# Optimization experiments

Measured on AMD Instinct MI355X. Metric: run time of the kernel, lower is better.

## Reference

```python
import jax, jax.numpy as jnp
import numpy as np

# Static DAG: input -> L hidden layers of K nodes (dense between layers) -> output.
B, WIDTH, K, L = 262144, 64, 4, 4


def _linear_init(key, shape, fan_in):
    # matches nn.Linear default: U(-1/sqrt(fan_in), 1/sqrt(fan_in))
    bound = 1.0 / np.sqrt(fan_in)
    return jax.random.uniform(key, shape, jnp.float32, -bound, bound)


def setup_inputs() -> dict:
    key = jax.random.key(0)
    ks = jax.random.split(key, 9)
    x = jax.random.normal(ks[0], (B, WIDTH), jnp.float32)
    # input node -> first hidden layer (K edges)
    W_in = _linear_init(ks[1], (K, WIDTH, WIDTH), WIDTH)
    b_in = _linear_init(ks[2], (K, WIDTH), WIDTH)
    # between hidden layers: (L-1) transitions, K*K edges each; [pred, node, out, in]
    W_mid = _linear_init(ks[3], (L - 1, K, K, WIDTH, WIDTH), WIDTH)
    b_mid = _linear_init(ks[4], (L - 1, K, K, WIDTH), WIDTH)
    # last hidden layer -> output node (K edges)
    W_out = _linear_init(ks[5], (K, WIDTH, WIDTH), WIDTH)
    b_out = _linear_init(ks[6], (K, WIDTH), WIDTH)
    return {"x": x, "W_in": W_in, "b_in": b_in, "W_mid": W_mid,
            "b_mid": b_mid, "W_out": W_out, "b_out": b_out}


def _l2_normalize(t):
    # torch.linalg.norm(t) with no dim: Frobenius norm over the WHOLE tensor
    return t / jnp.linalg.norm(t)


def reference(x, W_in, b_in, W_mid, b_mid, W_out, b_out):
    # input node -> layer 1: each node k gets a single edge Linear, then normalize
    h = jnp.einsum('bw,kvw->kbv', x, W_in) + b_in[:, None, :]  # [K,B,W]
    h = jax.vmap(_l2_normalize)(h)
    # hidden -> hidden transitions: node v sums over its K predecessor edges
    for l in range(L - 1):  # small fixed structural loop over layers
        pre = jnp.einsum('pbw,pkvw->kbv', h, W_mid[l]) + b_mid[l].sum(axis=0)[:, None, :]
        h = jax.vmap(_l2_normalize)(pre)
    # last layer -> output node: sum K edge outputs, normalize
    out = jnp.einsum('pbw,pvw->bv', h, W_out) + b_out.sum(axis=0)
    return _l2_normalize(out)
```

## Files before the change

kernel.cpp:

```cpp
#include <hip/hip_runtime.h>


#define BF 262144.0f

#define OFF_G     0
#define OFF_S     4096
#define OFF_Q1    4160
#define OFF_Q2    4224
#define OFF_Q3    4288
#define OFF_Q4    5312
#define OFF_N2    21696
#define OFF_COUT  21760
#define OFF_SV1   21824
#define OFF_SV2   22080
#define OFF_SV3   23104
#define OFF_SV4   27200
#define OFF_MO    43584
#define OFF_P2    49152
#define OFF_P3    114688
#define OFF_P4    376832
#define OFF_PO    1425408
#define OFF_X16   2473984
#define NZERO     17600

typedef __attribute__((ext_vector_type(8))) short bf16x8;
typedef __attribute__((ext_vector_type(4))) float f32x4;
typedef __attribute__((ext_vector_type(4))) unsigned short u16x4;

__device__ __forceinline__ unsigned short f2bf(float f) {
  unsigned u = __builtin_bit_cast(unsigned, f);
  u += 0x7FFF + ((u >> 16) & 1);
  return (unsigned short)(u >> 16);
}

__device__ __forceinline__ bf16x8 cvt8(f32x4 a, f32x4 b, float s) {
  bf16x8 t;
#pragma unroll
  for (int j = 0; j < 4; j++) {
    t[j]     = (short)f2bf(a[j] * s);
    t[j + 4] = (short)f2bf(b[j] * s);
  }
  return t;
}

__device__ __forceinline__ void ld64(float* dst, const float* __restrict__ src, int tid) {
#pragma unroll
  for (int m = 0; m < 4; m++) {
    const int li = m * 1024 + tid * 4;
    *(f32x4*)&dst[(li >> 6) * 68 + (li & 63)] = *(const f32x4*)(src + li);
  }
}
__device__ __forceinline__ void st64(float* __restrict__ dst, const float* src, int tid) {
#pragma unroll
  for (int m = 0; m < 4; m++) {
    const int li = m * 1024 + tid * 4;
    *(f32x4*)(dst + li) = *(const f32x4*)&src[(li >> 6) * 68 + (li & 63)];
  }
}
__device__ __forceinline__ void mm64(float* C, const float* A, const float* B, int tid) {
  const int v0 = (tid >> 4) * 4, w0 = (tid & 15) * 4;
  f32x4 a0 = {0.f,0.f,0.f,0.f}, a1 = a0, a2 = a0, a3 = a0;
#pragma unroll 8
  for (int u = 0; u < 64; u++) {
    const f32x4 b = *(const f32x4*)&B[u * 68 + w0];
    a0 += b * A[(v0 + 0) * 68 + u];
    a1 += b * A[(v0 + 1) * 68 + u];
    a2 += b * A[(v0 + 2) * 68 + u];
    a3 += b * A[(v0 + 3) * 68 + u];
  }
  *(f32x4*)&C[(v0 + 0) * 68 + w0] = a0;
  *(f32x4*)&C[(v0 + 1) * 68 + w0] = a1;
  *(f32x4*)&C[(v0 + 2) * 68 + w0] = a2;
  *(f32x4*)&C[(v0 + 3) * 68 + w0] = a3;
}

__global__ __launch_bounds__(256) void kGP(const float* __restrict__ x,
                                           float* __restrict__ Gpart,
                                           unsigned short* __restrict__ x16,
                                           const float* __restrict__ Win,
                                           const float* __restrict__ Wmid,
                                           const float* __restrict__ Wout,
                                           float* __restrict__ ws) {
  __shared__ __align__(16) char shm[3 * 4352 * 4];
  const int tid = threadIdx.x;

  if (blockIdx.x < 512) {
    typedef unsigned short xts_t[4][16][8];
    xts_t* xts = (xts_t*)shm;
    float (*sred)[4] = (float(*)[4])(shm + 4096);
    const int lane = tid & 63, mt = tid >> 6;
    const int col = lane & 15, q = lane >> 4;
    const int row0 = tid >> 4;
    const int cf0  = (tid & 15) * 4;

    f32x4 acc[4];
#pragma unroll
    for (int nt = 0; nt < 4; nt++) acc[nt] = (f32x4){0.f, 0.f, 0.f, 0.f};
    float s0 = 0.f, s1 = 0.f, s2 = 0.f, s3 = 0.f;

    const long brow = (long)blockIdx.x * 512;
    const float* bx = x + brow * 64;
    f32x4 r0 = *(const f32x4*)(bx + tid * 4);
    f32x4 r1 = *(const f32x4*)(bx + 1024 + tid * 4);

    for (int c = 0; c < 16; c++) {
      __syncthreads();
      s0 += r0[0] + r1[0]; s1 += r0[1] + r1[1];
      s2 += r0[2] + r1[2]; s3 += r0[3] + r1[3];
      u16x4 h0, h1;
#pragma unroll
      for (int j = 0; j < 4; j++) {
        const int cf = cf0 + j;
        const unsigned short b0 = f2bf(r0[j]);
        const unsigned short b1 = f2bf(r1[j]);
        h0[j] = b0; h1[j] = b1;
        xts[cf >> 4][row0 >> 3][cf & 15][row0 & 7]        = b0;
        xts[cf >> 4][2 + (row0 >> 3)][cf & 15][row0 & 7]  = b1;
      }
      *(u16x4*)(x16 + (brow + c * 32 + row0) * 64 + cf0)      = h0;
      *(u16x4*)(x16 + (brow + c * 32 + 16 + row0) * 64 + cf0) = h1;
      f32x4 r0n = r0, r1n = r1;
      if (c < 15) {
        r0n = *(const f32x4*)(bx + (c + 1) * 2048 + tid * 4);
        r1n = *(const f32x4*)(bx + (c + 1) * 2048 + 1024 + tid * 4);
      }
      __syncthreads();
      const bf16x8 af = *(const bf16x8*)xts[mt][q][col];
#pragma unroll
      for (int nt = 0; nt < 4; nt++) {
        const bf16x8 bfr = *(const bf16x8*)xts[nt][q][col];
        acc[nt] = __builtin_amdgcn_mfma_f32_16x16x32_bf16(af, bfr, acc[nt], 0, 0, 0);
      }
      r0 = r0n; r1 = r1n;
    }

    float* myp = Gpart + (long)blockIdx.x * 4160;
#pragma unroll
    for (int nt = 0; nt < 4; nt++)
#pragma unroll
      for (int r = 0; r < 4; r++)
        myp[(mt * 16 + q * 4 + r) * 64 + nt * 16 + col] = acc[nt][r];

    sred[tid][0] = s0; sred[tid][1] = s1; sred[tid][2] = s2; sred[tid][3] = s3;
    __syncthreads();
    if (tid < 64) {
      float t = 0.f;
#pragma unroll
      for (int k2 = 0; k2 < 16; k2++) t += sred[(tid >> 2) + 16 * k2][tid & 3];
      myp[4096 + tid] = t;
    }
  } else {
    float* mb0 = (float*)shm;
    float* mb1 = mb0 + 4352;
    float* mb2 = mb1 + 4352;
    const int pid = blockIdx.x - 512;
    const int p1 = (pid >> 6) & 3, p2 = (pid >> 4) & 3, p3 = (pid >> 2) & 3, p4 = pid & 3;
    ld64(mb0, Win + p1 * 4096, tid);
    ld64(mb1, Wmid + (p1 * 4 + p2) * 4096, tid);
    __syncthreads();
    mm64(mb2, mb1, mb0, tid);
    __syncthreads();
    if (p3 == 0 && p4 == 0) st64(ws + OFF_P2 + (p1 * 4 + p2) * 4096, mb2, tid);
    ld64(mb1, Wmid + 65536 + (p2 * 4 + p3) * 4096, tid);
    __syncthreads();
    mm64(mb0, mb1, mb2, tid);
    __syncthreads();
    if (p4 == 0) st64(ws + OFF_P3 + (p1 * 16 + p2 * 4 + p3) * 4096, mb0, tid);
    ld64(mb1, Wmid + 131072 + (p3 * 4 + p4) * 4096, tid);
    __syncthreads();
    mm64(mb2, mb1, mb0, tid);
    __syncthreads();
    st64(ws + OFF_P4 + pid * 4096, mb2, tid);
    ld64(mb1, Wout + p4 * 4096, tid);
    __syncthreads();
    mm64(mb0, mb1, mb2, tid);
    __syncthreads();
    st64(ws + OFF_PO + pid * 4096, mb0, tid);
  }
}

__global__ __launch_bounds__(256) void kGred(const float* __restrict__ Gpart,
                                             float* __restrict__ ws) {
  __shared__ float red[4][64];
  const int tid = threadIdx.x;
  for (int i = blockIdx.x * 256 + tid; i < NZERO; i += 65 * 256)
    ws[OFF_Q1 + i] = 0.f;
  const int e = blockIdx.x * 64 + (tid & 63);
  const int quarter = tid >> 6;
  float acc = 0.f;
#pragma unroll 4
  for (int j = 0; j < 128; j++)
    acc += Gpart[(long)(quarter * 128 + j) * 4160 + e];
  red[quarter][tid & 63] = acc;
  __syncthreads();
  if (tid < 64) {
    const float t = red[0][tid] + red[1][tid] + red[2][tid] + red[3][tid];
    const int ee = blockIdx.x * 64 + tid;
    if (ee < 4096) ws[OFF_G + ee] = t;
    else           ws[OFF_S + ee - 4096] = t;
  }
}

__global__ __launch_bounds__(256) void kTab(const float* __restrict__ Win,
                                            float* __restrict__ ws) {
  __shared__ __align__(16) float Gl[64 * 68];
  __shared__ __align__(16) float Al[64 * 68];
  __shared__ __align__(16) float Bl[64 * 68];
  __shared__ float red[256];
  __shared__ float sl[64];
  const int tid = threadIdx.x, b = blockIdx.x;
  const int it = tid >> 6, lane = tid & 63;

  ld64(Gl, ws + OFF_G, tid);
  if (tid < 64) sl[tid] = ws[OFF_S + tid];
  __syncthreads();

  if (b < 4) {
    ld64(Al, Win + b * 4096, tid);
    __syncthreads();
    const int vq = it, w = lane;
    float part = 0.f;
    for (int m = 0; m < 16; m++) {
      const int v = vq + m * 4;
      float bw = 0.f;
#pragma unroll 8
      for (int wp = 0; wp < 64; wp++) bw += Al[v * 68 + wp] * Gl[wp * 68 + w];
      part += bw * Al[v * 68 + w];
    }
    red[tid] = part;
    __syncthreads();
    for (int st = 128; st > 0; st >>= 1) {
      if (tid < st) red[tid] += red[tid + st];
      __syncthreads();
    }
    if (tid == 0) ws[OFF_Q1 + b] = red[0];
  } else if (b < 164) {
    int NP, nv, v0, node, qoff;
    const float* Pbase;
    if (b < 20)      { NP = 4;  node = (b - 4)  >> 2; v0 = ((b - 4)  & 3) * 16; nv = 16; Pbase = ws + OFF_P2; qoff = OFF_Q2 + node * 16; }
    else if (b < 36) { NP = 16; node = (b - 20) >> 2; v0 = ((b - 20) & 3) * 16; nv = 16; Pbase = ws + OFF_P3; qoff = OFF_Q3 + node * 256; }
    else             { NP = 64; node = (b - 36) >> 5; v0 = ((b - 36) & 31) * 2; nv = 2;  Pbase = ws + OFF_P4; qoff = OFF_Q4 + node * 4096; }

    float q1acc = 0.f;
    f32x4 qq0 = {0.f,0.f,0.f,0.f}, qq1 = qq0, qq2 = qq0, qq3 = qq0;

    for (int vi = 0; vi < nv; vi++) {
      const int v = v0 + vi;
      __syncthreads();
      for (int e = tid * 4; e < NP * 64; e += 1024) {
        const int j = e >> 6, c = e & 63;
        *(f32x4*)&Al[j * 68 + c] = *(const f32x4*)(Pbase + (long)(j * 4 + node) * 4096 + v * 64 + c);
      }
      __syncthreads();
      if (NP == 64) {
        const int j = tid >> 2, w0 = (tid & 3) * 16;
        f32x4 a0 = {0.f,0.f,0.f,0.f}, a1 = a0, a2 = a0, a3 = a0;
#pragma unroll 8
        for (int wp = 0; wp < 64; wp++) {
          const float a = Al[j * 68 + wp];
          a0 += a * *(const f32x4*)&Gl[wp * 68 + w0];
          a1 += a * *(const f32x4*)&Gl[wp * 68 + w0 + 4];
          a2 += a * *(const f32x4*)&Gl[wp * 68 + w0 + 8];
          a3 += a * *(const f32x4*)&Gl[wp * 68 + w0 + 12];
        }
        *(f32x4*)&Bl[j * 68 + w0]      = a0;
        *(f32x4*)&Bl[j * 68 + w0 + 4]  = a1;
        *(f32x4*)&Bl[j * 68 + w0 + 8]  = a2;
        *(f32x4*)&Bl[j * 68 + w0 + 12] = a3;
      } else if (NP == 16) {
        const int j = tid >> 4, w0 = (tid & 15) * 4;
        f32x4 a0 = {0.f,0.f,0.f,0.f};
#pragma unroll 8
        for (int wp = 0; wp < 64; wp++)
          a0 += Al[j * 68 + wp] * *(const f32x4*)&Gl[wp * 68 + w0];
        *(f32x4*)&Bl[j * 68 + w0] = a0;
      } else {
        const int j = tid >> 6, w = tid & 63;
        float a0 = 0.f;
#pragma unroll 8
        for (int wp = 0; wp < 64; wp++) a0 += Al[j * 68 + wp] * Gl[wp * 68 + w];
        Bl[j * 68 + w] = a0;
      }
      __syncthreads();
      if (NP == 64) {
        const int j0 = (tid >> 4) * 4, jp = tid & 15;
#pragma unroll 4
        for (int w4 = 0; w4 < 16; w4++) {
          const f32x4 b0 = *(const f32x4*)&Bl[(j0 + 0) * 68 + w4 * 4];
          const f32x4 b1 = *(const f32x4*)&Bl[(j0 + 1) * 68 + w4 * 4];
          const f32x4 b2 = *(const f32x4*)&Bl[(j0 + 2) * 68 + w4 * 4];
          const f32x4 b3 = *(const f32x4*)&Bl[(j0 + 3) * 68 + w4 * 4];
#pragma unroll
          for (int bb = 0; bb < 4; bb++) {
            const f32x4 av = *(const f32x4*)&Al[(jp + 16 * bb) * 68 + w4 * 4];
            qq0[bb] += b0[0]*av[0] + b0[1]*av[1] + b0[2]*av[2] + b0[3]*av[3];
            qq1[bb] += b1[0]*av[0] + b1[1]*av[1] + b1[2]*av[2] + b1[3]*av[3];
            qq2[bb] += b2[0]*av[0] + b2[1]*av[1] + b2[2]*av[2] + b2[3]*av[3];
            qq3[bb] += b3[0]*av[0] + b3[1]*av[1] + b3[2]*av[2] + b3[3]*av[3];
          }
        }
      } else if (NP == 16) {
        const int j = tid >> 4, jp = tid & 15;
#pragma unroll 4
        for (int w4 = 0; w4 < 16; w4++) {
          const f32x4 bv = *(const f32x4*)&Bl[j * 68 + w4 * 4];
          const f32x4 av = *(const f32x4*)&Al[jp * 68 + w4 * 4];
          q1acc += bv[0]*av[0] + bv[1]*av[1] + bv[2]*av[2] + bv[3]*av[3];
        }
      } else {
        if (tid < 16) {
          const int j = tid >> 2, jp = tid & 3;
#pragma unroll 8
          for (int w = 0; w < 64; w++) q1acc += Bl[j * 68 + w] * Al[jp * 68 + w];
        }
      }
    }
    if (NP == 64) {
      const int j0 = (tid >> 4) * 4, jp = tid & 15;
#pragma unroll
      for (int bb = 0; bb < 4; bb++) {
        atomicAdd(&ws[qoff + (j0 + 0) * 64 + jp + 16 * bb], qq0[bb]);
        atomicAdd(&ws[qoff + (j0 + 1) * 64 + jp + 16 * bb], qq1[bb]);
        atomicAdd(&ws[qoff + (j0 + 2) * 64 + jp + 16 * bb], qq2[bb]);
        atomicAdd(&ws[qoff + (j0 + 3) * 64 + jp + 16 * bb], qq3[bb]);
      }
    } else if (NP == 16) {
      atomicAdd(&ws[qoff + (tid >> 4) * 16 + (tid & 15)], q1acc);
    } else if (tid < 16) {
      atomicAdd(&ws[qoff + tid], q1acc);
    }
  } else {
    const int vb = b - 164;
    const int lo = vb * 85, hi = (vb == 3) ? 340 : lo + 85;
    for (int vec = lo + it; vec < hi; vec += 4) {
      const float* mat; int dst;
      if (vec < 4)       { mat = Win + vec * 4096;                dst = OFF_SV1 + vec * 64; }
      else if (vec < 20) { mat = ws + OFF_P2 + (vec - 4) * 4096;  dst = OFF_SV2 + (vec - 4) * 64; }
      else if (vec < 84) { mat = ws + OFF_P3 + (vec - 20) * 4096; dst = OFF_SV3 + (vec - 20) * 64; }
      else               { mat = ws + OFF_P4 + (vec - 84) * 4096; dst = OFF_SV4 + (vec - 84) * 64; }
      float acc = 0.f;
#pragma unroll
      for (int u4 = 0; u4 < 16; u4++) {
        const f32x4 mv = *(const f32x4*)(mat + lane * 64 + u4 * 4);
        acc += mv[0]*sl[u4*4] + mv[1]*sl[u4*4+1] + mv[2]*sl[u4*4+2] + mv[3]*sl[u4*4+3];
      }
      ws[dst + lane] = acc;
    }
  }
}

__global__ __launch_bounds__(256) void kLM(
    const float* __restrict__ bin, const float* __restrict__ Wmid,
    const float* __restrict__ bmid, const float* __restrict__ Wout,
    const float* __restrict__ bout, float* __restrict__ ws) {
  __shared__ float binl[256], c2l[256], c3l[256], c4l[256], col[64];
  __shared__ float sv1l[256], sv2l[1024];
  __shared__ float inv1[4], inv2[4], inv3[4], inv4[4];
  __shared__ float C2l[4], C3l[16], C4l[64], mco[256];
  __shared__ __align__(16) float Grow[64 * 68];
  __shared__ float sl[64];
  __shared__ float tfl[4][64];
  __shared__ float redb[256];
  const int tid = threadIdx.x, it = tid >> 6, lane = tid & 63;

  binl[tid] = bin[tid];
  sv1l[tid] = ws[OFF_SV1 + tid];
#pragma unroll
  for (int m = 0; m < 4; m++) sv2l[m * 256 + tid] = ws[OFF_SV2 + m * 256 + tid];
  if (tid < 64) sl[tid] = ws[OFF_S + tid];
  ld64(Grow, ws + OFF_G, tid);
  __syncthreads();

  {
    const float c = binl[it * 64 + lane];
    float part = c * (2.f * sv1l[it * 64 + lane] + BF * c);
#pragma unroll
    for (int off = 32; off; off >>= 1) part += __shfl_down(part, off, 64);
    if (lane == 0) inv1[it] = rsqrtf(ws[OFF_Q1 + it] + part);
  }
  __syncthreads();
  if (tid < 4) C2l[tid] = inv1[tid];
  __syncthreads();
  {
    float acc = 0.f;
#pragma unroll
    for (int src = 0; src < 4; src++) {
      const float* wr = Wmid + (long)((src * 4 + it) * 64 + lane) * 64;
      float pc = 0.f;
#pragma unroll
      for (int u4 = 0; u4 < 16; u4++) {
        const f32x4 wv = *(const f32x4*)(wr + u4 * 4);
        pc += wv[0]*binl[src*64+u4*4]   + wv[1]*binl[src*64+u4*4+1]
            + wv[2]*binl[src*64+u4*4+2] + wv[3]*binl[src*64+u4*4+3];
      }
      acc += inv1[src] * pc + bmid[(src * 4 + it) * 64 + lane];
    }
    c2l[it * 64 + lane] = acc;
  }
  __syncthreads();
  {
    float ts = 0.f;
#pragma unroll
    for (int p1 = 0; p1 < 4; p1++) ts += C2l[p1] * sv2l[(p1 * 4 + it) * 64 + lane];
    const float c = c2l[it * 64 + lane];
    float part = c * (2.f * ts + BF * c);
    if (lane < 16) part += C2l[lane >> 2] * C2l[lane & 3] * ws[OFF_Q2 + it * 16 + lane];
#pragma unroll
    for (int off = 32; off; off >>= 1) part += __shfl_down(part, off, 64);
    if (lane == 0) inv2[it] = rsqrtf(part);
  }
  __syncthreads();
  if (tid < 16) C3l[tid] = C2l[tid >> 2] * inv2[tid & 3];
  __syncthreads();
  {
    float acc = 0.f;
#pragma unroll
    for (int src = 0; src < 4; src++) {
      const float* wr = Wmid + 65536 + (long)((src * 4 + it) * 64 + lane) * 64;
      float pc = 0.f;
#pragma unroll
      for (int u4 = 0; u4 < 16; u4++) {
        const f32x4 wv = *(const f32x4*)(wr + u4 * 4);
        pc += wv[0]*c2l[src*64+u4*4]   + wv[1]*c2l[src*64+u4*4+1]
            + wv[2]*c2l[src*64+u4*4+2] + wv[3]*c2l[src*64+u4*4+3];
      }
      acc += inv2[src] * pc + bmid[1024 + (src * 4 + it) * 64 + lane];
    }
    c3l[it * 64 + lane] = acc;
  }
  __syncthreads();
  {
    float ts = 0.f;
#pragma unroll
    for (int j = 0; j < 16; j++) ts += C3l[j] * ws[OFF_SV3 + (j * 4 + it) * 64 + lane];
    const float c = c3l[it * 64 + lane];
    float part = c * (2.f * ts + BF * c);
#pragma unroll
    for (int k = 0; k < 4; k++) {
      const int idx = lane * 4 + k;
      part += C3l[idx >> 4] * C3l[idx & 15] * ws[OFF_Q3 + it * 256 + idx];
    }
#pragma unroll
    for (int off = 32; off; off >>= 1) part += __shfl_down(part, off, 64);
    if (lane == 0) inv3[it] = rsqrtf(part);
  }
  __syncthreads();
  if (tid < 64) C4l[tid] = C3l[tid >> 2] * inv3[tid & 3];
  __syncthreads();
  {
    float acc = 0.f;
#pragma unroll
    for (int src = 0; src < 4; src++) {
      const float* wr = Wmid + 131072 + (long)((src * 4 + it) * 64 + lane) * 64;
      float pc = 0.f;
#pragma unroll
      for (int u4 = 0; u4 < 16; u4++) {
        const f32x4 wv = *(const f32x4*)(wr + u4 * 4);
        pc += wv[0]*c3l[src*64+u4*4]   + wv[1]*c3l[src*64+u4*4+1]
            + wv[2]*c3l[src*64+u4*4+2] + wv[3]*c3l[src*64+u4*4+3];
      }
      acc += inv3[src] * pc + bmid[2048 + (src * 4 + it) * 64 + lane];
    }
    c4l[it * 64 + lane] = acc;
  }
  __syncthreads();
  {
    float ts = 0.f;
    for (int j = 0; j < 64; j++) ts += C4l[j] * ws[OFF_SV4 + (j * 4 + it) * 64 + lane];
    const float c = c4l[it * 64 + lane];
    float part = c * (2.f * ts + BF * c);
    float rsum = 0.f;
    const float* qrow = ws + OFF_Q4 + it * 4096 + lane * 64;
#pragma unroll 8
    for (int jp = 0; jp < 64; jp++) rsum += C4l[jp] * qrow[jp];
    part += C4l[lane] * rsum;
#pragma unroll
    for (int off = 32; off; off >>= 1) part += __shfl_down(part, off, 64);
    if (lane == 0) inv4[it] = rsqrtf(part);
  }
  __syncthreads();
  mco[tid] = C4l[tid >> 2] * inv4[tid & 3];
  {
    const float* wr = Wout + (long)(it * 64 + lane) * 64;
    float pc = 0.f;
#pragma unroll
    for (int u4 = 0; u4 < 16; u4++) {
      const f32x4 wv = *(const f32x4*)(wr + u4 * 4);
      pc += wv[0]*c4l[it*64+u4*4]   + wv[1]*c4l[it*64+u4*4+1]
          + wv[2]*c4l[it*64+u4*4+2] + wv[3]*c4l[it*64+u4*4+3];
    }
    c2l[it * 64 + lane] = inv4[it] * pc + bout[it * 64 + lane];
  }
  __syncthreads();
  if (tid < 64) col[tid] = c2l[tid] + c2l[64 + tid] + c2l[128 + tid] + c2l[192 + tid];
  __syncthreads();
  if (blockIdx.x == 0 && tid < 64) ws[OFF_COUT + tid] = col[tid];

  const int v = blockIdx.x * 4 + it;
  {
    float acc = 0.f;
    const float* po = ws + OFF_PO + v * 64 + lane;
#pragma unroll 4
    for (int i = 0; i < 256; i++) acc += mco[i] * po[(long)i * 4096];
    tfl[it][lane] = acc;
    ws[OFF_MO + v * 64 + lane] = acc;
  }
  __syncthreads();
  {
    float bw = 0.f;
#pragma unroll 8
    for (int wp = 0; wp < 64; wp++) bw += tfl[it][wp] * Grow[wp * 68 + lane];
    float part = bw * tfl[it][lane] + 2.f * col[v] * tfl[it][lane] * sl[lane];
    redb[tid] = part;
    __syncthreads();
    for (int st = 128; st > 0; st >>= 1) {
      if (tid < st) redb[tid] += redb[tid + st];
      __syncthreads();
    }
    if (tid == 0) atomicAdd(&ws[OFF_N2], redb[0]);
    if (blockIdx.x == 0 && it == 0) {
      float p2_ = BF * col[lane] * col[lane];
#pragma unroll
      for (int off = 32; off; off >>= 1) p2_ += __shfl_down(p2_, off, 64);
      if (lane == 0) atomicAdd(&ws[OFF_N2], p2_);
    }
  }
}

__global__ __launch_bounds__(256) void kApply(const unsigned short* __restrict__ x16,
                                              const float* __restrict__ MoU,
                                              const float* __restrict__ coU,
                                              const float* __restrict__ n2p,
                                              float* __restrict__ out) {
  const int tid = threadIdx.x, lane = tid & 63, vt = tid >> 6;
  const int col = lane & 15, q = lane >> 4;
  const float inv = rsqrtf(n2p[0]);

  bf16x8 bfr[2];
  const float* mr = MoU + (vt * 16 + col) * 64 + q * 8;
  bfr[0] = cvt8(*(const f32x4*)mr, *(const f32x4*)(mr + 4), inv);
  bfr[1] = cvt8(*(const f32x4*)(mr + 32), *(const f32x4*)(mr + 36), inv);
  const float cf = inv * coU[vt * 16 + col];

  for (int t = 0; t < 16; t++) {
    const int b0 = (blockIdx.x * 16 + t) * 16;
    const unsigned short* xr = x16 + (long)(b0 + col) * 64 + q * 8;
    const bf16x8 a0 = *(const bf16x8*)xr;
    const bf16x8 a1 = *(const bf16x8*)(xr + 32);
    f32x4 acc = (f32x4){0.f, 0.f, 0.f, 0.f};
    acc = __builtin_amdgcn_mfma_f32_16x16x32_bf16(a0, bfr[0], acc, 0, 0, 0);
    acc = __builtin_amdgcn_mfma_f32_16x16x32_bf16(a1, bfr[1], acc, 0, 0, 0);
#pragma unroll
    for (int r = 0; r < 4; r++)
      out[(long)(b0 + q * 4 + r) * 64 + vt * 16 + col] = acc[r] + cf;
  }
}

extern "C" void kernel_launch(void* const* d_in, const int* in_sizes, int n_in,
                              void* d_out, int out_size, void* d_ws, size_t ws_size,
                              hipStream_t stream) {
  const float* x    = (const float*)d_in[0];
  const float* Win  = (const float*)d_in[1];
  const float* bin  = (const float*)d_in[2];
  const float* Wmid = (const float*)d_in[3];
  const float* bmid = (const float*)d_in[4];
  const float* Wout = (const float*)d_in[5];
  const float* bout = (const float*)d_in[6];
  float* out = (float*)d_out;
  float* ws  = (float*)d_ws;
  float* Gpart = out;
  unsigned short* x16 = (unsigned short*)(ws + OFF_X16);

  kGP  <<<768, 256, 0, stream>>>(x, Gpart, x16, Win, Wmid, Wout, ws);
  kGred<<<65, 256, 0, stream>>>(Gpart, ws);
  kTab <<<168, 256, 0, stream>>>(Win, ws);
  kLM  <<<16, 256, 0, stream>>>(bin, Wmid, bmid, Wout, bout, ws);
  kApply<<<1024, 256, 0, stream>>>(x16, ws + OFF_MO, ws + OFF_COUT, ws + OFF_N2, out);
}
```

Baseline: 252.0 us.

## Precompute bias-propagation vectors in product kernel to shorten serial norm chain

The weight-product blocks of kGP now also compute matrix-vector products of the loaded weight tiles with the input biases and the propagated summed biases (u, v vectors) and store them in the workspace. kLM then builds each layer's constant vector as a small weighted sum of these precomputed vectors scaled by the norm factors, instead of doing 64-wide dot products against Wmid/Wout inside its serial chain. The Q4 reduction is also reordered to read coalesced columns. This moves work off the latency-bound 16-block kLM into the parallel kGP, at the cost of extra mv64 passes with syncthreads and more workspace writes in kGP.

```diff
diff --git a/kernel.cpp b/kernel.cpp
--- a/kernel.cpp
+++ b/kernel.cpp
@@ -16,11 +16,24 @@
 #define OFF_SV3   23104
 #define OFF_SV4   27200
 #define OFF_MO    43584
-#define OFF_P2    49152
-#define OFF_P3    114688
-#define OFF_P4    376832
-#define OFF_PO    1425408
-#define OFF_X16   2473984
+#define OFF_B0    47680
+#define OFF_B1    47936
+#define OFF_B2    48192
+#define OFF_U2    48512
+#define OFF_U3    49536
+#define OFF_U4    53632
+#define OFF_V3    70016
+#define OFF_V4A   71040
+#define OFF_V4B   75136
+#define OFF_UO    76160
+#define OFF_VOA   92544
+#define OFF_VOB   96640
+#define OFF_VOC   97664
+#define OFF_P2    98304
+#define OFF_P3    163840
+#define OFF_P4    425984
+#define OFF_PO    1474560
+#define OFF_X16   2523136
 #define NZERO     17600
 
 typedef __attribute__((ext_vector_type(8))) short bf16x8;
@@ -73,15 +86,30 @@
   *(f32x4*)&C[(v0 + 2) * 68 + w0] = a2;
   *(f32x4*)&C[(v0 + 3) * 68 + w0] = a3;
 }
+__device__ __forceinline__ void mv64(float* dst, const float* W, const float* vec,
+                                     float (*red)[64], int tid) {
+  const int v = tid & 63, q = tid >> 6;
+  float p = 0.f;
+#pragma unroll
+  for (int u = q * 16; u < q * 16 + 16; u++) p += W[v * 68 + u] * vec[u];
+  red[q][v] = p;
+  __syncthreads();
+  if (tid < 64) dst[tid] = red[0][tid] + red[1][tid] + red[2][tid] + red[3][tid];
+  __syncthreads();
+}
 
 __global__ __launch_bounds__(256) void kGP(const float* __restrict__ x,
                                            float* __restrict__ Gpart,
                                            unsigned short* __restrict__ x16,
                                            const float* __restrict__ Win,
+                                           const float* __restrict__ bin,
                                            const float* __restrict__ Wmid,
+                                           const float* __restrict__ bmid,
                                            const float* __restrict__ Wout,
                                            float* __restrict__ ws) {
   __shared__ __align__(16) char shm[3 * 4352 * 4];
+  __shared__ float vbuf[14][64];
+  __shared__ float red4v[4][64];
   const int tid = threadIdx.x;
 
   if (blockIdx.x < 512) {
@@ -153,29 +181,77 @@
     float* mb0 = (float*)shm;
     float* mb1 = mb0 + 4352;
     float* mb2 = mb1 + 4352;
+    float* binl = vbuf[0]; float* B0l = vbuf[1]; float* B1l = vbuf[2]; float* B2l = vbuf[3];
+    float* u2 = vbuf[4];  float* u3 = vbuf[5];  float* v3 = vbuf[6];
+    float* u4 = vbuf[7];  float* v4a = vbuf[8]; float* v4b = vbuf[9];
+    float* uo = vbuf[10]; float* voa = vbuf[11]; float* vob = vbuf[12]; float* voc = vbuf[13];
     const int pid = blockIdx.x - 512;
     const int p1 = (pid >> 6) & 3, p2 = (pid >> 4) & 3, p3 = (pid >> 2) & 3, p4 = pid & 3;
+    const float* bm0 = bmid;
+    const float* bm1 = bmid + 1024;
+    const float* bm2 = bmid + 2048;
+
+    if (tid < 64) {
+      binl[tid] = bin[p1 * 64 + tid];
+      B0l[tid] = bm0[(0*4+p2)*64+tid] + bm0[(1*4+p2)*64+tid] + bm0[(2*4+p2)*64+tid] + bm0[(3*4+p2)*64+tid];
+      B1l[tid] = bm1[(0*4+p3)*64+tid] + bm1[(1*4+p3)*64+tid] + bm1[(2*4+p3)*64+tid] + bm1[(3*4+p3)*64+tid];
+      B2l[tid] = bm2[(0*4+p4)*64+tid] + bm2[(1*4+p4)*64+tid] + bm2[(2*4+p4)*64+tid] + bm2[(3*4+p4)*64+tid];
+    }
     ld64(mb0, Win + p1 * 4096, tid);
     ld64(mb1, Wmid + (p1 * 4 + p2) * 4096, tid);
     __syncthreads();
+    mv64(u2, mb1, binl, red4v, tid);
     mm64(mb2, mb1, mb0, tid);
     __syncthreads();
-    if (p3 == 0 && p4 == 0) st64(ws + OFF_P2 + (p1 * 4 + p2) * 4096, mb2, tid);
+    if (p3 == 0 && p4 == 0) {
+      st64(ws + OFF_P2 + (p1 * 4 + p2) * 4096, mb2, tid);
+      if (tid < 64) ws[OFF_U2 + (p1 * 4 + p2) * 64 + tid] = u2[tid];
+    }
     ld64(mb1, Wmid + 65536 + (p2 * 4 + p3) * 4096, tid);
     __syncthreads();
+    mv64(u3, mb1, u2, red4v, tid);
+    mv64(v3, mb1, B0l, red4v, tid);
     mm64(mb0, mb1, mb2, tid);
     __syncthreads();
-    if (p4 == 0) st64(ws + OFF_P3 + (p1 * 16 + p2 * 4 + p3) * 4096, mb0, tid);
+    if (p4 == 0) {
+      st64(ws + OFF_P3 + (p1 * 16 + p2 * 4 + p3) * 4096, mb0, tid);
+      if (tid < 64) ws[OFF_U3 + (p1 * 16 + p2 * 4 + p3) * 64 + tid] = u3[tid];
+      if (p1 == 0 && tid < 64) ws[OFF_V3 + (p2 * 4 + p3) * 64 + tid] = v3[tid];
+    }
     ld64(mb1, Wmid + 131072 + (p3 * 4 + p4) * 4096, tid);
     __syncthreads();
+    mv64(u4, mb1, u3, red4v, tid);
+    mv64(v4a, mb1, v3, red4v, tid);
+    mv64(v4b, mb1, B1l, red4v, tid);
     mm64(mb2, mb1, mb0, tid);
     __syncthreads();
     st64(ws + OFF_P4 + pid * 4096, mb2, tid);
+    if (tid < 64) {
+      ws[OFF_U4 + pid * 64 + tid] = u4[tid];
+      if (p1 == 0) ws[OFF_V4A + ((p2 * 4 + p3) * 4 + p4) * 64 + tid] = v4a[tid];
+      if (p1 == 0 && p2 == 0) ws[OFF_V4B + (p3 * 4 + p4) * 64 + tid] = v4b[tid];
+    }
     ld64(mb1, Wout + p4 * 4096, tid);
     __syncthreads();
+    mv64(uo, mb1, u4, red4v, tid);
+    mv64(voa, mb1, v4a, red4v, tid);
+    mv64(vob, mb1, v4b, red4v, tid);
+    mv64(voc, mb1, B2l, red4v, tid);
     mm64(mb0, mb1, mb2, tid);
     __syncthreads();
     st64(ws + OFF_PO + pid * 4096, mb0, tid);
+    if (tid < 64) {
+      ws[OFF_UO + pid * 64 + tid] = uo[tid];
+      if (p1 == 0) ws[OFF_VOA + ((p2 * 4 + p3) * 4 + p4) * 64 + tid] = voa[tid];
+      if (p1 == 0 && p2 == 0) ws[OFF_VOB + (p3 * 4 + p4) * 64 + tid] = vob[tid];
+      if (p1 == 0 && p2 == 0 && p3 == 0) ws[OFF_VOC + p4 * 64 + tid] = voc[tid];
+    }
+    if (pid == 0) {
+      const int t = tid >> 6, v = tid & 63;
+      ws[OFF_B0 + tid] = bm0[(0*4+t)*64+v] + bm0[(1*4+t)*64+v] + bm0[(2*4+t)*64+v] + bm0[(3*4+t)*64+v];
+      ws[OFF_B1 + tid] = bm1[(0*4+t)*64+v] + bm1[(1*4+t)*64+v] + bm1[(2*4+t)*64+v] + bm1[(3*4+t)*64+v];
+      ws[OFF_B2 + tid] = bm2[(0*4+t)*64+v] + bm2[(1*4+t)*64+v] + bm2[(2*4+t)*64+v] + bm2[(3*4+t)*64+v];
+    }
   }
 }
 
@@ -350,9 +426,8 @@
 }
 
 __global__ __launch_bounds__(256) void kLM(
-    const float* __restrict__ bin, const float* __restrict__ Wmid,
-    const float* __restrict__ bmid, const float* __restrict__ Wout,
-    const float* __restrict__ bout, float* __restrict__ ws) {
+    const float* __restrict__ bin, const float* __restrict__ bout,
+    float* __restrict__ ws) {
   __shared__ float binl[256], c2l[256], c3l[256], c4l[256], col[64];
   __shared__ float sv1l[256], sv2l[1024];
   __shared__ float inv1[4], inv2[4], inv3[4], inv4[4];
@@ -382,19 +457,10 @@
   if (tid < 4) C2l[tid] = inv1[tid];
   __syncthreads();
   {
-    float acc = 0.f;
-#pragma unroll
-    for (int src = 0; src < 4; src++) {
-      const float* wr = Wmid + (long)((src * 4 + it) * 64 + lane) * 64;
-      float pc = 0.f;
-#pragma unroll
-      for (int u4 = 0; u4 < 16; u4++) {
-        const f32x4 wv = *(const f32x4*)(wr + u4 * 4);
-        pc += wv[0]*binl[src*64+u4*4]   + wv[1]*binl[src*64+u4*4+1]
-            + wv[2]*binl[src*64+u4*4+2] + wv[3]*binl[src*64+u4*4+3];
-      }
-      acc += inv1[src] * pc + bmid[(src * 4 + it) * 64 + lane];
-    }
+    float acc = ws[OFF_B0 + it * 64 + lane];
+#pragma unroll
+    for (int p1 = 0; p1 < 4; p1++)
+      acc += inv1[p1] * ws[OFF_U2 + (p1 * 4 + it) * 64 + lane];
     c2l[it * 64 + lane] = acc;
   }
   __syncthreads();
@@ -413,18 +479,14 @@
   if (tid < 16) C3l[tid] = C2l[tid >> 2] * inv2[tid & 3];
   __syncthreads();
   {
-    float acc = 0.f;
-#pragma unroll
-    for (int src = 0; src < 4; src++) {
-      const float* wr = Wmid + 65536 + (long)((src * 4 + it) * 64 + lane) * 64;
-      float pc = 0.f;
-#pragma unroll
-      for (int u4 = 0; u4 < 16; u4++) {
-        const f32x4 wv = *(const f32x4*)(wr + u4 * 4);
-        pc += wv[0]*c2l[src*64+u4*4]   + wv[1]*c2l[src*64+u4*4+1]
-            + wv[2]*c2l[src*64+u4*4+2] + wv[3]*c2l[src*64+u4*4+3];
-      }
-      acc += inv2[src] * pc + bmid[1024 + (src * 4 + it) * 64 + lane];
+    float acc = ws[OFF_B1 + it * 64 + lane];
+#pragma unroll
+    for (int p2 = 0; p2 < 4; p2++) {
+      float tmp = ws[OFF_V3 + (p2 * 4 + it) * 64 + lane];
+#pragma unroll
+      for (int p1 = 0; p1 < 4; p1++)
+        tmp += inv1[p1] * ws[OFF_U3 + ((p1 * 4 + p2) * 4 + it) * 64 + lane];
+      acc += inv2[p2] * tmp;
     }
     c3l[it * 64 + lane] = acc;
   }
@@ -448,18 +510,19 @@
   if (tid < 64) C4l[tid] = C3l[tid >> 2] * inv3[tid & 3];
   __syncthreads();
   {
-    float acc = 0.f;
-#pragma unroll
-    for (int src = 0; src < 4; src++) {
-      const float* wr = Wmid + 131072 + (long)((src * 4 + it) * 64 + lane) * 64;
-      float pc = 0.f;
-#pragma unroll
-      for (int u4 = 0; u4 < 16; u4++) {
-        const f32x4 wv = *(const f32x4*)(wr + u4 * 4);
-        pc += wv[0]*c3l[src*64+u4*4]   + wv[1]*c3l[src*64+u4*4+1]
-            + wv[2]*c3l[src*64+u4*4+2] + wv[3]*c3l[src*64+u4*4+3];
-      }
-      acc += inv3[src] * pc + bmid[2048 + (src * 4 + it) * 64 + lane];
+    float acc = ws[OFF_B2 + it * 64 + lane];
+#pragma unroll
+    for (int p3 = 0; p3 < 4; p3++) {
+      float t3 = ws[OFF_V4B + (p3 * 4 + it) * 64 + lane];
+#pragma unroll
+      for (int p2 = 0; p2 < 4; p2++) {
+        float t2 = ws[OFF_V4A + ((p2 * 4 + p3) * 4 + it) * 64 + lane];
+#pragma unroll
+        for (int p1 = 0; p1 < 4; p1++)
+          t2 += inv1[p1] * ws[OFF_U4 + (((p1 * 4 + p2) * 4 + p3) * 4 + it) * 64 + lane];
+        t3 += inv2[p2] * t2;
+      }
+      acc += inv3[p3] * t3;
     }
     c4l[it * 64 + lane] = acc;
   }
@@ -469,11 +532,11 @@
     for (int j = 0; j < 64; j++) ts += C4l[j] * ws[OFF_SV4 + (j * 4 + it) * 64 + lane];
     const float c = c4l[it * 64 + lane];
     float part = c * (2.f * ts + BF * c);
-    float rsum = 0.f;
-    const float* qrow = ws + OFF_Q4 + it * 4096 + lane * 64;
-#pragma unroll 8
-    for (int jp = 0; jp < 64; jp++) rsum += C4l[jp] * qrow[jp];
-    part += C4l[lane] * rsum;
+    float colv = 0.f;
+#pragma unroll 8
+    for (int j = 0; j < 64; j++)
+      colv += C4l[j] * ws[OFF_Q4 + it * 4096 + j * 64 + lane];
+    part += C4l[lane] * colv;
 #pragma unroll
     for (int off = 32; off; off >>= 1) part += __shfl_down(part, off, 64);
     if (lane == 0) inv4[it] = rsqrtf(part);
@@ -481,15 +544,21 @@
   __syncthreads();
   mco[tid] = C4l[tid >> 2] * inv4[tid & 3];
   {
-    const float* wr = Wout + (long)(it * 64 + lane) * 64;
-    float pc = 0.f;
-#pragma unroll
-    for (int u4 = 0; u4 < 16; u4++) {
-      const f32x4 wv = *(const f32x4*)(wr + u4 * 4);
-      pc += wv[0]*c4l[it*64+u4*4]   + wv[1]*c4l[it*64+u4*4+1]
-          + wv[2]*c4l[it*64+u4*4+2] + wv[3]*c4l[it*64+u4*4+3];
-    }
-    c2l[it * 64 + lane] = inv4[it] * pc + bout[it * 64 + lane];
+    float acc = ws[OFF_VOC + it * 64 + lane];
+#pragma unroll
+    for (int p3 = 0; p3 < 4; p3++) {
+      float t3 = ws[OFF_VOB + (p3 * 4 + it) * 64 + lane];
+#pragma unroll
+      for (int p2 = 0; p2 < 4; p2++) {
+        float t2 = ws[OFF_VOA + ((p2 * 4 + p3) * 4 + it) * 64 + lane];
+#pragma unroll
+        for (int p1 = 0; p1 < 4; p1++)
+          t2 += inv1[p1] * ws[OFF_UO + (((p1 * 4 + p2) * 4 + p3) * 4 + it) * 64 + lane];
+        t3 += inv2[p2] * t2;
+      }
+      acc += inv3[p3] * t3;
+    }
+    c2l[it * 64 + lane] = inv4[it] * acc + bout[it * 64 + lane];
   }
   __syncthreads();
   if (tid < 64) col[tid] = c2l[tid] + c2l[64 + tid] + c2l[128 + tid] + c2l[192 + tid];
@@ -571,9 +640,9 @@
   float* Gpart = out;
   unsigned short* x16 = (unsigned short*)(ws + OFF_X16);
 
-  kGP  <<<768, 256, 0, stream>>>(x, Gpart, x16, Win, Wmid, Wout, ws);
+  kGP  <<<768, 256, 0, stream>>>(x, Gpart, x16, Win, bin, Wmid, bmid, Wout, ws);
   kGred<<<65, 256, 0, stream>>>(Gpart, ws);
   kTab <<<168, 256, 0, stream>>>(Win, ws);
-  kLM  <<<16, 256, 0, stream>>>(bin, Wmid, bmid, Wout, bout, ws);
+  kLM  <<<16, 256, 0, stream>>>(bin, bout, ws);
   kApply<<<1024, 256, 0, stream>>>(x16, ws + OFF_MO, ws + OFF_COUT, ws + OFF_N2, out);
 }
```

After: 242.6 us. -3.7%, faster.
